# Performance work log

Hardware: AMD Instinct MI355X
Metric: run time of the kernel (lower is better)

The kernel has to match this reference:

```python
import jax, jax.numpy as jnp
import numpy as np

N = 100000          # number of nodes (queries == sources here)
DEG = 32            # uniform neighbor count
E = N * DEG         # total edges
C_IN = 8
HID = 32
C_OUT = 32


def setup_inputs() -> dict:
    key = jax.random.key(0)
    k1, k2, k3, k4, k5 = jax.random.split(key, 5)
    in_features = jax.random.normal(k1, (N, C_IN), dtype=jnp.float32)
    in_weights = jax.random.uniform(k2, (N,), dtype=jnp.float32)
    # MLP: Linear(2*C_IN -> HID), GELU, Linear(HID -> C_OUT)
    W1 = jax.random.normal(k3, (2 * C_IN, HID), dtype=jnp.float32) / np.sqrt(2 * C_IN)
    b1 = jnp.zeros((HID,), dtype=jnp.float32)
    W2 = jax.random.normal(k4, (HID, C_OUT), dtype=jnp.float32) / np.sqrt(HID)
    b2 = jnp.zeros((C_OUT,), dtype=jnp.float32)
    neighbor_index = jax.random.randint(k5, (E,), 0, N, dtype=jnp.int64)
    row_splits = (jnp.arange(N + 1, dtype=jnp.int64) * DEG)  # uniform CSR splits
    return {"in_features": in_features, "in_weights": in_weights,
            "W1": W1, "b1": b1, "W2": W2, "b2": b2,
            "neighbor_index": neighbor_index, "row_splits": row_splits}


def reference(in_features, in_weights, W1, b1, W2, b2, neighbor_index, row_splits):
    num_edges = neighbor_index.shape[0]
    num_out = row_splits.shape[0] - 1  # M output nodes
    # segment id of each edge (== repeat_interleave of node ids by row counts)
    seg = jnp.searchsorted(row_splits, jnp.arange(num_edges), side="right") - 1
    gathered = in_features[neighbor_index]          # [E, C_in] neighbor gather
    self_feats = in_features[seg]                   # [E, C_in] repeated self features
    agg = jnp.concatenate([gathered, self_feats], axis=1)  # [E, 2*C_in]
    h = jax.nn.gelu(agg @ W1 + b1)                  # [E, HID]
    h = h @ W2 + b2                                 # [E, C_out]
    h = in_weights[neighbor_index][:, None] * h     # quadrature weighting
    sums = jax.ops.segment_sum(h, seg, num_segments=num_out)  # segment_csr sum
    counts = (row_splits[1:] - row_splits[:-1]).astype(h.dtype)
    out = sums / jnp.maximum(counts, 1)[:, None]    # reduce='mean'
    return out
```

## Files before the change

kernel.cpp:

```cpp
#include <hip/hip_runtime.h>

#define DEG 32
#define HID 32
#define CIN 8

typedef float v2f __attribute__((ext_vector_type(2)));
typedef short bf16x8 __attribute__((ext_vector_type(8)));
typedef float f32x16 __attribute__((ext_vector_type(16)));

#define GELU_A ((float)(2.0 * 1.4426950408889634 * 0.7978845608028654))
#define GELU_B ((float)(2.0 * 1.4426950408889634 * 0.7978845608028654 * 0.044715))

__device__ __forceinline__ unsigned f2bf(float f) {
    unsigned b = __float_as_uint(f);
    return (b + 0x7fffu + ((b >> 16) & 1u)) >> 16;
}
__device__ __forceinline__ unsigned pack2(float lo, float hi) {
    return f2bf(lo) | (f2bf(hi) << 16);
}

__global__ __launch_bounds__(256) void precompute_xw(
    const float* __restrict__ x, const float* __restrict__ W1,
    const float* __restrict__ W2, unsigned* __restrict__ x16,
    unsigned* __restrict__ w1f, unsigned* __restrict__ w2f, int N) {
    int tid = blockIdx.x * 256 + threadIdx.x;
    if (blockIdx.x == 0) {
        int t = threadIdx.x;
        if (t < 64) {
            int kb = (t >> 5) * 8, col = t & 31;
            uint4 o;
            o.x = pack2(W1[(kb + 0) * HID + col], W1[(kb + 1) * HID + col]);
            o.y = pack2(W1[(kb + 2) * HID + col], W1[(kb + 3) * HID + col]);
            o.z = pack2(W1[(kb + 4) * HID + col], W1[(kb + 5) * HID + col]);
            o.w = pack2(W1[(kb + 6) * HID + col], W1[(kb + 7) * HID + col]);
            *(uint4*)(w1f + t * 4) = o;
        } else if (t < 192) {
            int u = t - 64;
            int f = u >> 6, l = u & 63;
            int kb = f * 16 + ((l >> 5) * 8), col = l & 31;
            uint4 o;
            o.x = pack2(W2[(kb + 0) * HID + col], W2[(kb + 1) * HID + col]);
            o.y = pack2(W2[(kb + 2) * HID + col], W2[(kb + 3) * HID + col]);
            o.z = pack2(W2[(kb + 4) * HID + col], W2[(kb + 5) * HID + col]);
            o.w = pack2(W2[(kb + 6) * HID + col], W2[(kb + 7) * HID + col]);
            *(uint4*)(w2f + (f * 64 + l) * 4) = o;
        }
    }
    if (tid < N) {
        const float4* xp = (const float4*)(x + (size_t)tid * CIN);
        float4 a = xp[0], b = xp[1];
        uint4 o;
        o.x = pack2(a.x, a.y);  o.y = pack2(a.z, a.w);
        o.z = pack2(b.x, b.y);  o.w = pack2(b.z, b.w);
        *(uint4*)(x16 + (size_t)tid * 4) = o;
    }
}

__device__ __forceinline__ float gelu_reduce(const f32x16& acc, const float* swp,
                                             float b1v) {
    v2f gacc = {0.f, 0.f};
#pragma unroll
    for (int q = 0; q < 4; ++q) {
        float4 wq = *(const float4*)(swp + 8 * q);
#pragma unroll
        for (int h = 0; h < 2; ++h) {
            int i = q * 4 + h * 2;
            v2f tt = {acc[i] + b1v, acc[i + 1] + b1v};
            v2f x2 = tt * tt;
            v2f zz = tt * (x2 * (-GELU_B) + (-GELU_A));
            v2f ee;
            ee.x = __builtin_amdgcn_exp2f(zz.x);  ee.y = __builtin_amdgcn_exp2f(zz.y);
            v2f dd = ee + 1.0f;
            v2f rr;
            rr.x = __builtin_amdgcn_rcpf(dd.x);   rr.y = __builtin_amdgcn_rcpf(dd.y);
            v2f wp = h ? (v2f){wq.z, wq.w} : (v2f){wq.x, wq.y};
            gacc += wp * (tt * rr);
        }
    }
    float g = gacc.x + gacc.y;
    g += __shfl_xor(g, 32);
    return g;
}

__global__ __launch_bounds__(256, 4) void git_fused(
    const unsigned* __restrict__ x16, const unsigned* __restrict__ w1f,
    const unsigned* __restrict__ w2f, const float* __restrict__ wgt,
    const float* __restrict__ b1, const float* __restrict__ b2,
    const int* __restrict__ nbr, float* __restrict__ out, int N) {
    __shared__ float sw[4 * 4 * 32];
    __shared__ __align__(16) unsigned short sg[1792];

    int t = threadIdx.x;
    int wv = t >> 6;
    int l  = t & 63;
    int l5 = l & 31;
    int hi = l >> 5;
    int nb = blockIdx.x * 16 + wv * 4;

    int n0 = min(nb + 0, N - 1), n1 = min(nb + 1, N - 1);
    int n2 = min(nb + 2, N - 1), n3 = min(nb + 3, N - 1);

    int JA = nbr[(hi ? n1 : n0) * DEG + l5];
    int JB = nbr[(hi ? n3 : n2) * DEG + l5];
    float WA = wgt[JA];
    float WB = wgt[JB];
    int jswA = __shfl_xor(JA, 32);
    int jswB = __shfl_xor(JB, 32);

    const bf16x8* x16v = (const bf16x8*)x16;
    bf16x8 A0 = x16v[hi ? n0 : JA];
    bf16x8 A1 = x16v[hi ? n1 : jswA];
    bf16x8 A2 = x16v[hi ? n2 : JB];
    bf16x8 A3 = x16v[hi ? n3 : jswB];
    bf16x8 bfrag = *((const bf16x8*)w1f + l);
    bf16x8 eb1   = *((const bf16x8*)w2f + l);
    bf16x8 eb2   = *((const bf16x8*)w2f + 64 + l);
    float myb1 = b1[l5];
    float myb2 = b2[l5];

    float* swv = &sw[wv * 128];
    swv[hi * 32 + l5]      = WA;
    swv[64 + hi * 32 + l5] = WB;

    float wsA = WA, wsB = WB;
    wsA += __shfl_xor(wsA, 1);  wsA += __shfl_xor(wsA, 2);
    wsA += __shfl_xor(wsA, 4);  wsA += __shfl_xor(wsA, 8);
    wsA += __shfl_xor(wsA, 16);
    wsB += __shfl_xor(wsB, 1);  wsB += __shfl_xor(wsB, 2);
    wsB += __shfl_xor(wsB, 4);  wsB += __shfl_xor(wsB, 8);
    wsB += __shfl_xor(wsB, 16);

    f32x16 z0 = {}, z1 = {};
    f32x16 a0 = __builtin_amdgcn_mfma_f32_32x32x16_bf16(A0, bfrag, z0, 0, 0, 0);
    f32x16 a1 = __builtin_amdgcn_mfma_f32_32x32x16_bf16(A1, bfrag, z1, 0, 0, 0);
    float g0 = gelu_reduce(a0, swv + hi * 4,      myb1);
    float g1 = gelu_reduce(a1, swv + 32 + hi * 4, myb1);
    f32x16 z2 = {}, z3 = {};
    f32x16 a2 = __builtin_amdgcn_mfma_f32_32x32x16_bf16(A2, bfrag, z2, 0, 0, 0);
    f32x16 a3 = __builtin_amdgcn_mfma_f32_32x32x16_bf16(A3, bfrag, z3, 0, 0, 0);
    float g2 = gelu_reduce(a2, swv + 64 + hi * 4, myb1);
    float g3 = gelu_reduce(a3, swv + 96 + hi * 4, myb1);

    unsigned short* sgw = &sg[wv * 160];
    float ga = hi ? g2 : g0;
    float gb = hi ? g3 : g1;
    sgw[(2 * hi + 0) * 40 + l5] = (unsigned short)f2bf(ga);
    sgw[(2 * hi + 1) * 40 + l5] = (unsigned short)f2bf(gb);

    float wsa[4];
    wsa[0] = __shfl(wsA, 0);
    wsa[1] = __shfl(wsA, 32);
    wsa[2] = __shfl(wsB, 0);
    wsa[3] = __shfl(wsB, 32);

    const char* sgb = (const char*)sgw;
    bf16x8 ea1 = *(const bf16x8*)(sgb + l5 * 80 + hi * 16);
    bf16x8 ea2 = *(const bf16x8*)(sgb + l5 * 80 + 32 + hi * 16);
    f32x16 zz = {};
    f32x16 acc = __builtin_amdgcn_mfma_f32_32x32x16_bf16(ea1, eb1, zz, 0, 0, 0);
    acc = __builtin_amdgcn_mfma_f32_32x32x16_bf16(ea2, eb2, acc, 0, 0, 0);

    if (hi == 0) {
#pragma unroll
        for (int i = 0; i < 4; ++i) {
            int node = nb + i;
            if (node < N)
                out[(size_t)node * HID + l5] =
                    fmaf(wsa[i], myb2, acc[i]) * (1.0f / DEG);
        }
    }
}

__global__ __launch_bounds__(256) void fused_fallback(
    const float* __restrict__ x, const float* __restrict__ wgt,
    const float* __restrict__ W1, const float* __restrict__ b1,
    const float* __restrict__ W2, const float* __restrict__ b2,
    const int* __restrict__ nbr, float* __restrict__ out, int N) {
    __shared__ float sW2[HID * HID];
    __shared__ float sb2[HID];
    __shared__ int2  sp[8 * DEG];
    int t = threadIdx.x;
#pragma unroll
    for (int i = 0; i < 4; ++i) sW2[t + i * 256] = W2[t + i * 256];
    if (t < HID) sb2[t] = b2[t];
    int slot = t >> 5, hid = t & 31;
    int node = blockIdx.x * 8 + slot;
    bool valid = node < N;
    int nc = valid ? node : (N - 1);
    int   j_own = nbr[nc * DEG + hid];
    float w_own = wgt[j_own];
    sp[slot * DEG + hid] = make_int2(j_own * (CIN * 4), __float_as_int(w_own));
    const float4* xip = (const float4*)(x + (size_t)nc * CIN);
    float4 xa = xip[0], xb = xip[1];
    float w1t[8];
#pragma unroll
    for (int k = 0; k < 8; ++k) w1t[k] = W1[k * HID + hid];
    float vb = b1[hid];
    vb = fmaf(xa.x, W1[ 8 * HID + hid], vb);
    vb = fmaf(xa.y, W1[ 9 * HID + hid], vb);
    vb = fmaf(xa.z, W1[10 * HID + hid], vb);
    vb = fmaf(xa.w, W1[11 * HID + hid], vb);
    vb = fmaf(xb.x, W1[12 * HID + hid], vb);
    vb = fmaf(xb.y, W1[13 * HID + hid], vb);
    vb = fmaf(xb.z, W1[14 * HID + hid], vb);
    vb = fmaf(xb.w, W1[15 * HID + hid], vb);
    float ws = w_own;
    ws += __shfl_xor(ws, 1);  ws += __shfl_xor(ws, 2);
    ws += __shfl_xor(ws, 4);  ws += __shfl_xor(ws, 8);
    ws += __shfl_xor(ws, 16);
    __syncthreads();
    const char* xbytes = (const char*)x;
    const int2* myp = &sp[slot * DEG];
    float g = 0.f;
#pragma unroll 8
    for (int e = 0; e < DEG; ++e) {
        int2  p  = myp[e];
        float wjv = __int_as_float(p.y);
        const float4* xjp = (const float4*)(xbytes + (unsigned)p.x);
        float4 a = xjp[0], b = xjp[1];
        float tin = vb;
        tin = fmaf(a.x, w1t[0], tin); tin = fmaf(a.y, w1t[1], tin);
        tin = fmaf(a.z, w1t[2], tin); tin = fmaf(a.w, w1t[3], tin);
        tin = fmaf(b.x, w1t[4], tin); tin = fmaf(b.y, w1t[5], tin);
        tin = fmaf(b.z, w1t[6], tin); tin = fmaf(b.w, w1t[7], tin);
        float x2 = tin * tin;
        float z  = tin * fmaf(GELU_B, x2, GELU_A);
        float e2 = __builtin_amdgcn_exp2f(z);
        float r  = __builtin_amdgcn_rcpf(1.0f + e2);
        g = fmaf(wjv, fmaf(-tin, r, tin), g);
    }
    float acc = 0.f;
#pragma unroll
    for (int h = 0; h < HID; ++h) {
        float gh = __shfl(g, h, 32);
        acc = fmaf(gh, sW2[h * HID + hid], acc);
    }
    if (valid) out[(size_t)node * HID + hid] = fmaf(ws, sb2[hid], acc) * (1.0f / DEG);
}

extern "C" void kernel_launch(void* const* d_in, const int* in_sizes, int n_in,
                              void* d_out, int out_size, void* d_ws, size_t ws_size,
                              hipStream_t stream) {
    const float* x   = (const float*)d_in[0];
    const float* wq  = (const float*)d_in[1];
    const float* W1  = (const float*)d_in[2];
    const float* b1  = (const float*)d_in[3];
    const float* W2  = (const float*)d_in[4];
    const float* b2  = (const float*)d_in[5];
    const int*   nbr = (const int*)d_in[6];
    float* out = (float*)d_out;

    int N = in_sizes[1];

    size_t off_x16 = 0;
    size_t off_w1  = (off_x16 + (size_t)N * 16 + 255) & ~(size_t)255;
    size_t off_w2  = off_w1 + 1024;
    size_t need    = off_w2 + 2048;

    if (ws_size >= need) {
        unsigned* x16 = (unsigned*)((char*)d_ws + off_x16);
        unsigned* w1f = (unsigned*)((char*)d_ws + off_w1);
        unsigned* w2f = (unsigned*)((char*)d_ws + off_w2);

        int blocks_pre = (N + 255) / 256;
        precompute_xw<<<blocks_pre, 256, 0, stream>>>(x, W1, W2, x16, w1f, w2f, N);

        int blocks_main = (N + 15) / 16;
        git_fused<<<blocks_main, 256, 0, stream>>>(x16, w1f, w2f, wq, b1, b2,
                                                   nbr, out, N);
    } else {
        int blocks = (N + 7) / 8;
        fused_fallback<<<blocks, 256, 0, stream>>>(x, wq, W1, b1, W2, b2, nbr, out, N);
    }
}
```

Before: 115.8 us.

## Split fused kernel into gather/GELU kernel and separate W2 MFMA epilogue

Splits the fused kernel into two launches. The first gathers neighbours, runs the W1 MFMA and the weighted GELU reduction for two nodes per wave, and writes bf16 partial sums and weight sums to workspace. A second kernel reads those rows back and applies W2 with a full 32-node MFMA tile per wave, replacing the mostly wasted 4-row MFMA in the old kernel. This removes shared-memory staging and halves per-wave register state, but adds an extra launch and a global-memory round trip for the intermediate data.

```diff
diff --git a/kernel.cpp b/kernel.cpp
--- a/kernel.cpp
+++ b/kernel.cpp
@@ -82,92 +82,83 @@
     return g;
 }
 
-__global__ __launch_bounds__(256, 4) void git_fused(
+__global__ __launch_bounds__(256) void git_fused_g(
     const unsigned* __restrict__ x16, const unsigned* __restrict__ w1f,
-    const unsigned* __restrict__ w2f, const float* __restrict__ wgt,
-    const float* __restrict__ b1, const float* __restrict__ b2,
-    const int* __restrict__ nbr, float* __restrict__ out, int N) {
-    __shared__ float sw[4 * 4 * 32];
-    __shared__ __align__(16) unsigned short sg[1792];
+    const float* __restrict__ wgt, const float* __restrict__ b1,
+    const int* __restrict__ nbr, unsigned short* __restrict__ gws,
+    float* __restrict__ wsum, int N) {
+    __shared__ float sw[4 * 64];
 
     int t = threadIdx.x;
     int wv = t >> 6;
     int l  = t & 63;
     int l5 = l & 31;
     int hi = l >> 5;
-    int nb = blockIdx.x * 16 + wv * 4;
+    int nb = blockIdx.x * 8 + wv * 2;
 
     int n0 = min(nb + 0, N - 1), n1 = min(nb + 1, N - 1);
-    int n2 = min(nb + 2, N - 1), n3 = min(nb + 3, N - 1);
-
-    int JA = nbr[(hi ? n1 : n0) * DEG + l5];
-    int JB = nbr[(hi ? n3 : n2) * DEG + l5];
-    float WA = wgt[JA];
-    float WB = wgt[JB];
-    int jswA = __shfl_xor(JA, 32);
-    int jswB = __shfl_xor(JB, 32);
+
+    int   J = nbr[(hi ? n1 : n0) * DEG + l5];
+    float W = wgt[J];
+    int jsw = __shfl_xor(J, 32);
 
     const bf16x8* x16v = (const bf16x8*)x16;
-    bf16x8 A0 = x16v[hi ? n0 : JA];
-    bf16x8 A1 = x16v[hi ? n1 : jswA];
-    bf16x8 A2 = x16v[hi ? n2 : JB];
-    bf16x8 A3 = x16v[hi ? n3 : jswB];
+    bf16x8 A0 = x16v[hi ? n0 : J];
+    bf16x8 A1 = x16v[hi ? n1 : jsw];
     bf16x8 bfrag = *((const bf16x8*)w1f + l);
-    bf16x8 eb1   = *((const bf16x8*)w2f + l);
-    bf16x8 eb2   = *((const bf16x8*)w2f + 64 + l);
     float myb1 = b1[l5];
-    float myb2 = b2[l5];
-
-    float* swv = &sw[wv * 128];
-    swv[hi * 32 + l5]      = WA;
-    swv[64 + hi * 32 + l5] = WB;
-
-    float wsA = WA, wsB = WB;
-    wsA += __shfl_xor(wsA, 1);  wsA += __shfl_xor(wsA, 2);
-    wsA += __shfl_xor(wsA, 4);  wsA += __shfl_xor(wsA, 8);
-    wsA += __shfl_xor(wsA, 16);
-    wsB += __shfl_xor(wsB, 1);  wsB += __shfl_xor(wsB, 2);
-    wsB += __shfl_xor(wsB, 4);  wsB += __shfl_xor(wsB, 8);
-    wsB += __shfl_xor(wsB, 16);
+
+    float* swv = &sw[wv * 64];
+    swv[hi * 32 + l5] = W;
+
+    float ws = W;
+    ws += __shfl_xor(ws, 1);  ws += __shfl_xor(ws, 2);
+    ws += __shfl_xor(ws, 4);  ws += __shfl_xor(ws, 8);
+    ws += __shfl_xor(ws, 16);
 
     f32x16 z0 = {}, z1 = {};
     f32x16 a0 = __builtin_amdgcn_mfma_f32_32x32x16_bf16(A0, bfrag, z0, 0, 0, 0);
     f32x16 a1 = __builtin_amdgcn_mfma_f32_32x32x16_bf16(A1, bfrag, z1, 0, 0, 0);
+
     float g0 = gelu_reduce(a0, swv + hi * 4,      myb1);
     float g1 = gelu_reduce(a1, swv + 32 + hi * 4, myb1);
-    f32x16 z2 = {}, z3 = {};
-    f32x16 a2 = __builtin_amdgcn_mfma_f32_32x32x16_bf16(A2, bfrag, z2, 0, 0, 0);
-    f32x16 a3 = __builtin_amdgcn_mfma_f32_32x32x16_bf16(A3, bfrag, z3, 0, 0, 0);
-    float g2 = gelu_reduce(a2, swv + 64 + hi * 4, myb1);
-    float g3 = gelu_reduce(a3, swv + 96 + hi * 4, myb1);
-
-    unsigned short* sgw = &sg[wv * 160];
-    float ga = hi ? g2 : g0;
-    float gb = hi ? g3 : g1;
-    sgw[(2 * hi + 0) * 40 + l5] = (unsigned short)f2bf(ga);
-    sgw[(2 * hi + 1) * 40 + l5] = (unsigned short)f2bf(gb);
-
-    float wsa[4];
-    wsa[0] = __shfl(wsA, 0);
-    wsa[1] = __shfl(wsA, 32);
-    wsa[2] = __shfl(wsB, 0);
-    wsa[3] = __shfl(wsB, 32);
-
-    const char* sgb = (const char*)sgw;
-    bf16x8 ea1 = *(const bf16x8*)(sgb + l5 * 80 + hi * 16);
-    bf16x8 ea2 = *(const bf16x8*)(sgb + l5 * 80 + 32 + hi * 16);
+
+    float ga   = hi ? g1 : g0;
+    int   node = hi ? n1 : n0;
+    gws[(size_t)node * HID + l5] = (unsigned short)f2bf(ga);
+    if (l5 == 0) wsum[node] = ws;
+}
+
+__global__ __launch_bounds__(256) void git_w2(
+    const unsigned short* __restrict__ gws, const unsigned* __restrict__ w2f,
+    const float* __restrict__ wsum, const float* __restrict__ b2,
+    float* __restrict__ out, int N) {
+    __shared__ float sws[4 * 32];
+
+    int t = threadIdx.x;
+    int wv = t >> 6, l = t & 63, l5 = l & 31, hi = l >> 5;
+    int nb = blockIdx.x * 128 + wv * 32;
+    int nl = min(nb + l5, N - 1);
+
+    const char* gb = (const char*)gws;
+    bf16x8 ea1 = *(const bf16x8*)(gb + (size_t)nl * 64 + hi * 16);
+    bf16x8 ea2 = *(const bf16x8*)(gb + (size_t)nl * 64 + 32 + hi * 16);
+    bf16x8 eb1 = *((const bf16x8*)w2f + l);
+    bf16x8 eb2 = *((const bf16x8*)w2f + 64 + l);
+    sws[wv * 32 + l5] = wsum[nl];
+    float myb2 = b2[l5];
+
     f32x16 zz = {};
     f32x16 acc = __builtin_amdgcn_mfma_f32_32x32x16_bf16(ea1, eb1, zz, 0, 0, 0);
     acc = __builtin_amdgcn_mfma_f32_32x32x16_bf16(ea2, eb2, acc, 0, 0, 0);
 
-    if (hi == 0) {
-#pragma unroll
-        for (int i = 0; i < 4; ++i) {
-            int node = nb + i;
-            if (node < N)
-                out[(size_t)node * HID + l5] =
-                    fmaf(wsa[i], myb2, acc[i]) * (1.0f / DEG);
-        }
+    const float* swsv = &sws[wv * 32];
+#pragma unroll
+    for (int i = 0; i < 16; ++i) {
+        int r = (i & 3) + 8 * (i >> 2) + 4 * hi;
+        int node = nb + r;
+        if (node < N)
+            out[(size_t)node * HID + l5] = fmaf(swsv[r], myb2, acc[i]) * (1.0f / DEG);
     }
 }
 
@@ -252,22 +243,29 @@
 
     int N = in_sizes[1];
 
-    size_t off_x16 = 0;
-    size_t off_w1  = (off_x16 + (size_t)N * 16 + 255) & ~(size_t)255;
-    size_t off_w2  = off_w1 + 1024;
-    size_t need    = off_w2 + 2048;
+    size_t off_x16  = 0;
+    size_t off_w1   = (off_x16 + (size_t)N * 16 + 255) & ~(size_t)255;
+    size_t off_w2   = off_w1 + 1024;
+    size_t off_g    = (off_w2 + 2048 + 255) & ~(size_t)255;
+    size_t off_wsum = (off_g + (size_t)N * HID * 2 + 255) & ~(size_t)255;
+    size_t need     = off_wsum + (size_t)N * 4;
 
     if (ws_size >= need) {
         unsigned* x16 = (unsigned*)((char*)d_ws + off_x16);
         unsigned* w1f = (unsigned*)((char*)d_ws + off_w1);
         unsigned* w2f = (unsigned*)((char*)d_ws + off_w2);
+        unsigned short* gws = (unsigned short*)((char*)d_ws + off_g);
+        float* wsum = (float*)((char*)d_ws + off_wsum);
 
         int blocks_pre = (N + 255) / 256;
         precompute_xw<<<blocks_pre, 256, 0, stream>>>(x, W1, W2, x16, w1f, w2f, N);
 
-        int blocks_main = (N + 15) / 16;
-        git_fused<<<blocks_main, 256, 0, stream>>>(x16, w1f, w2f, wq, b1, b2,
-                                                   nbr, out, N);
+        int blocks_main = (N + 7) / 8;
+        git_fused_g<<<blocks_main, 256, 0, stream>>>(x16, w1f, wq, b1, nbr,
+                                                     gws, wsum, N);
+
+        int blocks_ep = (N + 127) / 128;
+        git_w2<<<blocks_ep, 256, 0, stream>>>(gws, w2f, wsum, b2, out, N);
     } else {
         int blocks = (N + 7) / 8;
         fused_fallback<<<blocks, 256, 0, stream>>>(x, wq, W1, b1, W2, b2, nbr, out, N);
```

Result: slower. 120.6 us (+4.2%).
